# Performance work log

Measured on AMD Instinct MI355X. Metric: run time of the kernel, lower is better.

## Reference

```python
import jax, jax.numpy as jnp
import numpy as np
from jax import lax

# GlobalSeed with a standard Mamba2 (SSD) core.
# C=64 feature channels, G=8 token dim, d_inner=16, d_state=16, nheads=2, headdim=8, d_conv=3.
C_FEAT, G, D_INNER, D_STATE, NHEADS, HEADDIM, D_CONV = 64, 8, 16, 16, 2, 8, 3
CONV_DIM = D_INNER + 2 * D_STATE  # 48
D_IN_PROJ = 2 * D_INNER + 2 * D_STATE + NHEADS  # 66


def setup_inputs() -> dict:
    key = jax.random.key(0)
    ks = jax.random.split(key, 16)
    B, H, W = 16, 128, 128
    s = 0.02
    return {
        "x": jax.random.normal(ks[0], (B, C_FEAT, H, W), jnp.float32),
        "tok_w": s * jax.random.normal(ks[1], (G, C_FEAT), jnp.float32),
        "tok_b": jnp.zeros((G,), jnp.float32),
        "detok_w": s * jax.random.normal(ks[2], (C_FEAT, G), jnp.float32),
        "detok_b": jnp.zeros((C_FEAT,), jnp.float32),
        "in_proj_w": s * jax.random.normal(ks[3], (D_IN_PROJ, G), jnp.float32),
        "in_proj_b": jnp.zeros((D_IN_PROJ,), jnp.float32),
        "conv_w": s * jax.random.normal(ks[4], (CONV_DIM, D_CONV), jnp.float32),
        "conv_b": jnp.zeros((CONV_DIM,), jnp.float32),
        "A_log": jnp.log(jnp.arange(1, NHEADS + 1, dtype=jnp.float32)),
        "D": jnp.ones((NHEADS,), jnp.float32),
        "dt_bias": 0.1 * jax.random.normal(ks[5], (NHEADS,), jnp.float32),
        "norm_w": jnp.ones((D_INNER,), jnp.float32),
        "out_w": s * jax.random.normal(ks[6], (G, D_INNER), jnp.float32),
        "out_b": jnp.zeros((G,), jnp.float32),
    }


def _mamba2(gt, in_proj_w, in_proj_b, conv_w, conv_b, A_log, D, dt_bias, norm_w, out_w, out_b):
    # gt: (B, L, G) tokens
    B, L, _ = gt.shape
    zxbcdt = gt @ in_proj_w.T + in_proj_b  # (B, L, 66)
    z = zxbcdt[..., :D_INNER]
    xBC = zxbcdt[..., D_INNER:D_INNER + CONV_DIM]
    dt = zxbcdt[..., D_INNER + CONV_DIM:]  # (B, L, nheads)
    # depthwise causal conv1d over L
    xBC = lax.conv_general_dilated(
        xBC.transpose(0, 2, 1), conv_w[:, None, :], (1,), [(D_CONV - 1, 0)],
        feature_group_count=CONV_DIM).transpose(0, 2, 1) + conv_b
    xBC = jax.nn.silu(xBC)
    xr = xBC[..., :D_INNER].reshape(B, L, NHEADS, HEADDIM)
    Bm = xBC[..., D_INNER:D_INNER + D_STATE]   # (B, L, N)
    Cm = xBC[..., D_INNER + D_STATE:]          # (B, L, N)
    dt = jax.nn.softplus(dt + dt_bias)          # (B, L, H)
    dec = jnp.exp(dt * (-jnp.exp(A_log)))       # (B, L, H)

    def step(h, inp):
        xt, Bt, Ct, dtt, dct = inp  # (B,H,P) (B,N) (B,N) (B,H) (B,H)
        h = dct[:, :, None, None] * h + (dtt[:, :, None] * xt)[..., None] * Bt[:, None, None, :]
        y = jnp.einsum('bhpn,bn->bhp', h, Ct)
        return h, y

    h0 = jnp.zeros((B, NHEADS, HEADDIM, D_STATE), gt.dtype)
    xs = (xr.transpose(1, 0, 2, 3), Bm.transpose(1, 0, 2), Cm.transpose(1, 0, 2),
          dt.transpose(1, 0, 2), dec.transpose(1, 0, 2))
    _, ys = lax.scan(step, h0, xs)  # (L, B, H, P)
    y = ys.transpose(1, 0, 2, 3) + D[None, None, :, None] * xr
    y = y.reshape(B, L, D_INNER)
    y = y * jax.nn.silu(z)  # gated
    y = y * lax.rsqrt(jnp.mean(y * y, axis=-1, keepdims=True) + 1e-5) * norm_w  # RMSNormGated
    return y @ out_w.T + out_b  # (B, L, G)


def reference(x, tok_w, tok_b, detok_w, detok_b, in_proj_w, in_proj_b, conv_w, conv_b,
              A_log, D, dt_bias, norm_w, out_w, out_b):
    B, C, H, W = x.shape
    L = H * W
    g = jnp.einsum('bchw,gc->bghw', x, tok_w) + tok_b[None, :, None, None]
    gt = g.reshape(B, G, L).transpose(0, 2, 1)  # (B, L, G)
    gt = _mamba2(gt, in_proj_w, in_proj_b, conv_w, conv_b, A_log, D, dt_bias, norm_w, out_w, out_b) + gt
    g2 = gt.transpose(0, 2, 1).reshape(B, G, H, W)
    return x + jnp.einsum('bghw,cg->bchw', g2, detok_w) + detok_b[None, :, None, None]
```

## Files before the change

### kernel.cpp

```cpp
#include <hip/hip_runtime.h>
#include <math.h>

#define NB 16
#define CF 64
#define LL 16384
#define GG 8
#define NH 2
#define CHN 64
#define NCH 256
#define NGRP 16

static constexpr size_t OFF_GT = 0;
static constexpr size_t OFF_U2 = OFF_GT + (size_t)NB*LL*GG;
static constexpr size_t OFF_AC = OFF_U2 + (size_t)NB*NCH*256;
static constexpr size_t OFF_PH = OFF_AC + (size_t)NB*NCH*NH;
static constexpr size_t OFF_CP = OFF_PH + (size_t)NB*NCH*256;
static constexpr size_t OFF_UG = OFF_CP + (size_t)NB*NCH*NH;
static constexpr size_t OFF_AG = OFF_UG + (size_t)NB*NGRP*256;
static constexpr size_t OFF_GH = OFF_AG + (size_t)NB*NGRP*NH;
static constexpr size_t OFF_G2 = OFF_GH + (size_t)NB*NGRP*256;
static constexpr size_t OFF_ST = OFF_G2 + (size_t)NB*LL*GG;
static constexpr size_t WS_FLOATS = OFF_ST + (size_t)NB*NCH*1792;

typedef float f32x4 __attribute__((ext_vector_type(4)));
typedef short bf16x8 __attribute__((ext_vector_type(8)));

__device__ __forceinline__ float siluf(float v){ return v / (1.f + __expf(-v)); }
__device__ __forceinline__ float softplusf(float v){ return v > 20.f ? v : log1pf(__expf(v)); }

__device__ __forceinline__ unsigned short f2bf(float f){
    unsigned int u = __float_as_uint(f);
    u += 0x7fffu + ((u >> 16) & 1u);
    return (unsigned short)(u >> 16);
}
__device__ __forceinline__ float bf2f(unsigned short s){
    return __uint_as_float(((unsigned int)s) << 16);
}
__device__ __forceinline__ unsigned int pack2bf(float lo, float hi){
    return (unsigned int)f2bf(lo) | ((unsigned int)f2bf(hi) << 16);
}
__device__ __forceinline__ unsigned int packtr(float lo, float hi){
    return (__float_as_uint(hi) & 0xffff0000u) | (__float_as_uint(lo) >> 16);
}

__device__ __forceinline__ void load8(float* d, const float* p){
    float4 a = ((const float4*)p)[0];
    float4 b = ((const float4*)p)[1];
    d[0]=a.x; d[1]=a.y; d[2]=a.z; d[3]=a.w;
    d[4]=b.x; d[5]=b.y; d[6]=b.z; d[7]=b.w;
}

__global__ __launch_bounds__(64) void k1a_tok(
    const float* __restrict__ x, const float* __restrict__ tok_w,
    const float* __restrict__ tok_b, float* __restrict__ gtw)
{
    __shared__ float s_tok[GG*CF];
    int tid = threadIdx.x;
    int b  = blockIdx.x >> 6;
    int ck = blockIdx.x & 63;
    int l0 = (ck << 8) + (tid << 2);
    for (int i = tid; i < GG*CF; i += 64) s_tok[i] = tok_w[i];
    __syncthreads();
    float acc[4][GG];
    #pragma unroll
    for (int r = 0; r < 4; ++r)
        #pragma unroll
        for (int g = 0; g < GG; ++g) acc[r][g] = tok_b[g];
    const float* xb = x + (size_t)b*CF*LL + l0;
    #pragma unroll 8
    for (int c = 0; c < CF; ++c) {
        float4 xv = *(const float4*)(xb + (size_t)c*LL);
        float xa[4] = {xv.x, xv.y, xv.z, xv.w};
        #pragma unroll
        for (int g = 0; g < GG; ++g) {
            float w = s_tok[g*CF + c];
            #pragma unroll
            for (int r = 0; r < 4; ++r) acc[r][g] = fmaf(xa[r], w, acc[r][g]);
        }
    }
    float* gp = gtw + ((size_t)b*LL + l0)*GG;
    #pragma unroll
    for (int r = 0; r < 4; ++r) {
        ((float4*)gp)[r*2+0] = make_float4(acc[r][0],acc[r][1],acc[r][2],acc[r][3]);
        ((float4*)gp)[r*2+1] = make_float4(acc[r][4],acc[r][5],acc[r][6],acc[r][7]);
    }
}

__global__ __launch_bounds__(256) void k2a_state(
    const float* __restrict__ gtw,
    const float* __restrict__ ipw, const float* __restrict__ ipb,
    const float* __restrict__ cw, const float* __restrict__ cb,
    const float* __restrict__ A_log, const float* __restrict__ dt_bias,
    float* __restrict__ stw,
    float* __restrict__ U2w, float* __restrict__ Acw)
{
    __shared__ float s_pre[48*68];
    __shared__ float s_xf[64*17], s_bf[64*17], s_cf[64*17];
    __shared__ __align__(16) unsigned short WXbf[16*72];
    __shared__ __align__(16) unsigned short BTbf[16*72];
    __shared__ float s_dt[64][2], s_nda[64][2], s_w[64][2];
    __shared__ float s_ipw[384], s_ipb2[48], s_cw2[144], s_cb2[48], s_wdt[16];

    int tid = threadIdx.x;
    int b = blockIdx.x >> 8, c = blockIdx.x & 255;
    float* stp = stw + ((size_t)(b*NCH + c))*1792;
    for (int i = tid; i < 384; i += 256) s_ipw[i] = ipw[128 + i];
    if (tid < 48) { s_ipb2[tid] = ipb[16 + tid]; s_cb2[tid] = cb[tid]; }
    else if (tid >= 64 && tid < 208) s_cw2[tid - 64] = cw[tid - 64];
    else if (tid >= 224 && tid < 240) s_wdt[tid - 224] = ipw[512 + (tid - 224)];
    __syncthreads();

    float a0e = __expf(A_log[0]), a1e = __expf(A_log[1]);
    float dtb0 = dt_bias[0], dtb1 = dt_bias[1];
    float bdt0 = ipb[64], bdt1 = ipb[65];

    int r = tid >> 2, sub = tid & 3;
    int l = c*CHN + r;
    {
        float g0[8];
        load8(g0, gtw + ((size_t)b*LL + l)*GG);
        #pragma unroll
        for (int k = 0; k < 12; ++k) {
            int ch = sub*12 + k;
            float acc = s_ipb2[ch];
            #pragma unroll
            for (int g = 0; g < 8; ++g) acc = fmaf(g0[g], s_ipw[ch*8+g], acc);
            s_pre[ch*68 + r + 2] = acc;
        }
        if (r < 2) {
            int lh = c*CHN - 1 - r, slot = 1 - r;
            if (lh >= 0) {
                float gh[8];
                load8(gh, gtw + ((size_t)b*LL + lh)*GG);
                #pragma unroll
                for (int k = 0; k < 12; ++k) {
                    int ch = sub*12 + k;
                    float acc = s_ipb2[ch];
                    #pragma unroll
                    for (int g = 0; g < 8; ++g) acc = fmaf(gh[g], s_ipw[ch*8+g], acc);
                    s_pre[ch*68 + slot] = acc;
                }
            } else {
                #pragma unroll
                for (int k = 0; k < 12; ++k) s_pre[(sub*12+k)*68 + slot] = 0.f;
            }
        }
        if (sub == 0) {
            float d0 = bdt0, d1 = bdt1;
            #pragma unroll
            for (int g = 0; g < 8; ++g) {
                d0 = fmaf(g0[g], s_wdt[g],   d0);
                d1 = fmaf(g0[g], s_wdt[8+g], d1);
            }
            float dt0 = softplusf(d0 + dtb0), dt1 = softplusf(d1 + dtb1);
            s_dt[r][0] = dt0; s_dt[r][1] = dt1;
            s_nda[r][0] = -dt0*a0e; s_nda[r][1] = -dt1*a1e;
        }
    }
    __syncthreads();

    {
        #pragma unroll
        for (int k = 0; k < 12; ++k) {
            int ch = sub*12 + k;
            float p0 = s_pre[ch*68 + r];
            float p1 = s_pre[ch*68 + r + 1];
            float p2 = s_pre[ch*68 + r + 2];
            float a = s_cb2[ch];
            a = fmaf(p0, s_cw2[ch*3+0], a);
            a = fmaf(p1, s_cw2[ch*3+1], a);
            a = fmaf(p2, s_cw2[ch*3+2], a);
            float v = siluf(a);
            if (ch < 16)      s_xf[r*17 + ch] = v;
            else if (ch < 32) s_bf[r*17 + (ch-16)] = v;
            else              s_cf[r*17 + (ch-32)] = v;
        }
    }
    if (tid < 64) {
        int rr = tid;
        float v0 = s_nda[rr][0], v1 = s_nda[rr][1];
        #pragma unroll
        for (int off = 1; off < 64; off <<= 1) {
            float t0 = __shfl_up(v0, off);
            float t1 = __shfl_up(v1, off);
            if (rr >= off) { v0 += t0; v1 += t1; }
        }
        float f0 = __shfl(v0, 63), f1 = __shfl(v1, 63);
        s_w[rr][0] = __expf(f0 - v0) * s_dt[rr][0];
        s_w[rr][1] = __expf(f1 - v1) * s_dt[rr][1];
        stp[1536 + rr*2 + 0] = v0;
        stp[1536 + rr*2 + 1] = v1;
        stp[1664 + rr*2 + 0] = s_dt[rr][0];
        stp[1664 + rr*2 + 1] = s_dt[rr][1];
        if (rr == 63)
            *(float2*)(Acw + ((size_t)b*NCH + c)*2) = make_float2(__expf(f0), __expf(f1));
    }
    __syncthreads();

    {
        unsigned int* stX = (unsigned int*)stp;
        unsigned int* stB = (unsigned int*)(stp + 512);
        unsigned int* stC = (unsigned int*)(stp + 1024);
        int half = tid >> 7;
        int t2 = tid & 127;
        int p = t2 & 15, seg = t2 >> 4;
        if (half == 0) {
            unsigned int wdW[4], wdX[4];
            #pragma unroll
            for (int j = 0; j < 4; ++j) {
                int s0 = seg*8 + 2*j, s1 = s0 + 1;
                float x0 = s_xf[s0*17 + p], x1 = s_xf[s1*17 + p];
                wdX[j] = pack2bf(x0, x1);
                wdW[j] = pack2bf(x0 * s_w[s0][p>>3], x1 * s_w[s1][p>>3]);
            }
            *(uint4*)&WXbf[p*72 + seg*8] = make_uint4(wdW[0],wdW[1],wdW[2],wdW[3]);
            *(uint4*)&stX[p*32 + seg*4]  = make_uint4(wdX[0],wdX[1],wdX[2],wdX[3]);
        } else {
            unsigned int wd[4];
            #pragma unroll
            for (int j = 0; j < 4; ++j) {
                int s0 = seg*8 + 2*j, s1 = s0 + 1;
                wd[j] = pack2bf(s_bf[s0*17 + p], s_bf[s1*17 + p]);
            }
            *(uint4*)&BTbf[p*72 + seg*8] = make_uint4(wd[0],wd[1],wd[2],wd[3]);
            int r2 = t2 >> 1, hf = t2 & 1;
            unsigned int wb[4], wc[4];
            #pragma unroll
            for (int j = 0; j < 4; ++j) {
                int c0 = hf*8 + 2*j;
                wb[j] = pack2bf(s_bf[r2*17 + c0], s_bf[r2*17 + c0 + 1]);
                wc[j] = pack2bf(s_cf[r2*17 + c0], s_cf[r2*17 + c0 + 1]);
            }
            *(uint4*)&stB[r2*8 + hf*4] = make_uint4(wb[0],wb[1],wb[2],wb[3]);
            *(uint4*)&stC[r2*8 + hf*4] = make_uint4(wc[0],wc[1],wc[2],wc[3]);
        }
    }
    __syncthreads();

    if (tid < 64) {
        int ar = tid & 15, kb = tid >> 4;
        f32x4 acc = {0.f, 0.f, 0.f, 0.f};
        #pragma unroll
        for (int kk = 0; kk < 2; ++kk) {
            bf16x8 aw = *(const bf16x8*)&WXbf[ar*72 + kk*32 + kb*8];
            bf16x8 bb = *(const bf16x8*)&BTbf[ar*72 + kk*32 + kb*8];
            acc = __builtin_amdgcn_mfma_f32_16x16x32_bf16(aw, bb, acc, 0, 0, 0);
        }
        #pragma unroll
        for (int rg = 0; rg < 4; ++rg)
            U2w[(((size_t)b*NCH + c) << 8) + (kb*4+rg)*16 + ar] = acc[rg];
    }
}

__global__ void k4c1(const float* __restrict__ U2w, const float* __restrict__ Acw,
                     float* __restrict__ phw, float* __restrict__ cpw,
                     float* __restrict__ Ugw, float* __restrict__ Agw)
{
    int b = blockIdx.x >> 4, grp = blockIdx.x & 15;
    int e = threadIdx.x, he = e >> 7;
    size_t base = (size_t)b*NCH + grp*16;
    float u[16], A[16];
    #pragma unroll
    for (int j = 0; j < 16; ++j) u[j] = U2w[((base + j) << 8) + e];
    #pragma unroll
    for (int j = 0; j < 16; ++j) A[j] = Acw[(base + j)*2 + he];
    float h = 0.f, cp = 1.f;
    #pragma unroll
    for (int j = 0; j < 16; ++j) {
        phw[((base + j) << 8) + e] = h;
        if ((e & 127) == 0) cpw[(base + j)*2 + he] = cp;
        h = fmaf(A[j], h, u[j]);
        cp *= A[j];
    }
    Ugw[(((size_t)b*NGRP + grp) << 8) + e] = h;
    if ((e & 127) == 0) Agw[((size_t)b*NGRP + grp)*2 + he] = cp;
}

__global__ void k4c2(const float* __restrict__ Ugw, const float* __restrict__ Agw,
                     float* __restrict__ ghw)
{
    int b = blockIdx.x, e = threadIdx.x, he = e >> 7;
    float u[NGRP], ag[NGRP];
    #pragma unroll
    for (int g = 0; g < NGRP; ++g) {
        u[g]  = Ugw[(((size_t)b*NGRP + g) << 8) + e];
        ag[g] = Agw[((size_t)b*NGRP + g)*2 + he];
    }
    float h = 0.f;
    #pragma unroll
    for (int g = 0; g < NGRP; ++g) {
        ghw[(((size_t)b*NGRP + g) << 8) + e] = h;
        h = fmaf(ag[g], h, u[g]);
    }
}

__global__ __launch_bounds__(256) void k2b_fused(
    const float* __restrict__ gtw,
    const float* __restrict__ ipw, const float* __restrict__ ipb,
    const float* __restrict__ Dv, const float* __restrict__ norm_w,
    const float* __restrict__ out_w, const float* __restrict__ out_b,
    const float* __restrict__ phw, const float* __restrict__ cpw,
    const float* __restrict__ ghw, const float* __restrict__ stw,
    float* __restrict__ g2w)
{
    __shared__ union {
        unsigned short Ct[64*40];
        float yb[64*20];
    } uC;
    __shared__ __align__(16) unsigned short Bt[64*40];
    __shared__ __align__(16) unsigned short XTbf[16*72];
    __shared__ __align__(16) unsigned short M2[2][64*72];
    __shared__ __align__(16) unsigned short Cp0[64*16], Cp1[64*16];
    __shared__ __align__(16) unsigned short hinT[2][8*16];
    __shared__ float s_hin[256];
    __shared__ float s_la[128];
    __shared__ float s_eti[2][64], s_etd[2][64], s_esc[2][4][4];
    __shared__ float s_zw[128], s_ow[128], s_zb[16], s_nw[16], s_ob[8];

    int tid = threadIdx.x;
    int b = blockIdx.x >> 8, c = blockIdx.x & 255;
    const float* stp = stw + ((size_t)(b*NCH + c))*1792;
    const unsigned int* stX = (const unsigned int*)stp;
    const unsigned int* stB = (const unsigned int*)(stp + 512);
    const unsigned int* stC = (const unsigned int*)(stp + 1024);

    int r = tid >> 2, sub = tid & 3;
    float g0[8];
    load8(g0, gtw + ((size_t)b*LL + c*CHN + r)*GG);
    {
        int grp = c >> 4;
        float gh  = ghw[(((size_t)b*NGRP + grp) << 8) + tid];
        float cpv = cpw[((size_t)b*NCH + c)*2 + (tid >> 7)];
        float phv = phw[(((size_t)b*NCH + c) << 8) + tid];
        s_hin[tid] = fmaf(cpv, gh, phv);
    }
    if (tid < 64) {
        int row = tid;
        *(uint4*)&uC.Ct[row*40]      = *(const uint4*)&stC[row*8];
        *(uint4*)&uC.Ct[row*40 + 8]  = *(const uint4*)&stC[row*8 + 4];
        *(uint4*)&uC.Ct[row*40 + 16] = make_uint4(0,0,0,0);
        *(uint4*)&uC.Ct[row*40 + 24] = make_uint4(0,0,0,0);
    } else if (tid < 128) {
        int row = tid - 64;
        *(uint4*)&Bt[row*40]      = *(const uint4*)&stB[row*8];
        *(uint4*)&Bt[row*40 + 8]  = *(const uint4*)&stB[row*8 + 4];
        *(uint4*)&Bt[row*40 + 16] = make_uint4(0,0,0,0);
        *(uint4*)&Bt[row*40 + 24] = make_uint4(0,0,0,0);
    } else {
        int i = tid - 128;
        int p = i >> 3, seg = i & 7;
        *(uint4*)&XTbf[p*72 + seg*8] = *(const uint4*)&stX[p*32 + seg*4];
    }
    if (tid < 128) { s_la[tid] = stp[1536 + tid]; s_zw[tid] = ipw[tid]; }
    else s_ow[tid-128] = out_w[tid-128];
    if (tid < 16) { s_zb[tid] = ipb[tid]; s_nw[tid] = norm_w[tid]; }
    else if (tid < 24) s_ob[tid-16] = out_b[tid-16];
    __syncthreads();

    float D0 = Dv[0], D1 = Dv[1];
    int lane = tid & 63, wv = tid >> 6;
    int ar = lane & 15, kb = lane >> 4;
    int trow = wv*16 + kb*4;

    f32x4 gT[4];
    {
        bf16x8 aC = *(const bf16x8*)&uC.Ct[(wv*16 + ar)*40 + kb*8];
        #pragma unroll
        for (int ss = 0; ss < 4; ++ss) {
            f32x4 g = {0.f, 0.f, 0.f, 0.f};
            if (ss <= wv) {
                bf16x8 bB = *(const bf16x8*)&Bt[(ss*16 + ar)*40 + kb*8];
                g = __builtin_amdgcn_mfma_f32_16x16x32_bf16(aC, bB, g, 0, 0, 0);
            }
            gT[ss] = g;
        }
    }
    if (tid < 128) {
        int h = tid >> 6;
        int rr = (tid & 63);
        float sc = __expf(s_la[rr*2 + h]);
        unsigned short* Cp = h ? Cp1 : Cp0;
        unsigned int* dst = (unsigned int*)&Cp[rr*16];
        #pragma unroll
        for (int j = 0; j < 8; ++j)
            dst[j] = pack2bf(sc * bf2f(uC.Ct[rr*40 + j*2]),
                             sc * bf2f(uC.Ct[rr*40 + j*2 + 1]));
        if (tid < 32) {
            int i = tid;
            int hh = i >> 4, p = (i >> 1) & 7, half = i & 1;
            unsigned int wd[4];
            #pragma unroll
            for (int j = 0; j < 4; ++j)
                wd[j] = pack2bf(s_hin[hh*128 + p*16 + half*8 + 2*j],
                                s_hin[hh*128 + p*16 + half*8 + 2*j + 1]);
            *(uint4*)&hinT[hh][p*16 + half*8] = make_uint4(wd[0],wd[1],wd[2],wd[3]);
        }
    } else {
        int i = tid - 128;
        int h = i >> 6, s = i & 63;
        int anc = s & ~15;
        float d = s_la[anc*2 + h] - s_la[s*2 + h];
        float dtv = stp[1664 + s*2 + h];
        s_eti[h][s] = __expf(-d);
        s_etd[h][s] = __expf(d) * dtv;
        if (i < 32) {
            int h2 = i >> 4, wt = (i >> 2) & 3, ws = i & 3;
            s_esc[h2][wt][ws] = (wt >= ws) ?
                __expf(s_la[(wt*16)*2 + h2] - s_la[(ws*16)*2 + h2]) : 0.f;
        }
    }
    __syncthreads();

    {
        float rowf0[4], rowf1[4];
        #pragma unroll
        for (int rg = 0; rg < 4; ++rg) {
            rowf0[rg] = s_eti[0][trow+rg];
            rowf1[rg] = s_eti[1][trow+rg];
        }
        #pragma unroll
        for (int ss = 0; ss < 4; ++ss) {
            int s = ss*16 + ar;
            if (ss > wv) {
                if (!(ar & 1)) {
                    #pragma unroll
                    for (int rg = 0; rg < 4; ++rg) {
                        *(unsigned int*)&M2[0][(trow+rg)*72 + ss*16 + ar] = 0u;
                        *(unsigned int*)&M2[1][(trow+rg)*72 + ss*16 + ar] = 0u;
                    }
                }
                continue;
            }
            float colf0 = s_esc[0][wv][ss] * s_etd[0][s];
            float colf1 = s_esc[1][wv][ss] * s_etd[1][s];
            #pragma unroll
            for (int rg = 0; rg < 4; ++rg) {
                bool keep = (s <= trow+rg);
                float m0 = keep ? rowf0[rg]*colf0*gT[ss][rg] : 0.f;
                float m1 = keep ? rowf1[rg]*colf1*gT[ss][rg] : 0.f;
                float m0p = __shfl_xor(m0, 1);
                float m1p = __shfl_xor(m1, 1);
                if (!(ar & 1)) {
                    *(unsigned int*)&M2[0][(trow+rg)*72 + ss*16 + ar] = packtr(m0, m0p);
                    *(unsigned int*)&M2[1][(trow+rg)*72 + ss*16 + ar] = packtr(m1, m1p);
                }
            }
        }
    }
    __syncthreads();

    {
        int p = ar;
        f32x4 acc0 = {0.f,0.f,0.f,0.f}, acc1 = {0.f,0.f,0.f,0.f};
        #pragma unroll
        for (int kk = 0; kk < 2; ++kk) {
            bf16x8 am0 = *(const bf16x8*)&M2[0][(wv*16 + ar)*72 + kk*32 + kb*8];
            bf16x8 am1 = *(const bf16x8*)&M2[1][(wv*16 + ar)*72 + kk*32 + kb*8];
            bf16x8 bx0 = {0,0,0,0,0,0,0,0}, bx1 = {0,0,0,0,0,0,0,0};
            if (p < 8) {
                bx0 = *(const bf16x8*)&XTbf[p*72 + kk*32 + kb*8];
                bx1 = *(const bf16x8*)&XTbf[(8+p)*72 + kk*32 + kb*8];
            }
            acc0 = __builtin_amdgcn_mfma_f32_16x16x32_bf16(am0, bx0, acc0, 0, 0, 0);
            acc1 = __builtin_amdgcn_mfma_f32_16x16x32_bf16(am1, bx1, acc1, 0, 0, 0);
        }
        bf16x8 aCp0 = {0,0,0,0,0,0,0,0}, aCp1 = {0,0,0,0,0,0,0,0};
        bf16x8 bh0 = {0,0,0,0,0,0,0,0}, bh1 = {0,0,0,0,0,0,0,0};
        if (kb < 2) {
            aCp0 = *(const bf16x8*)&Cp0[(wv*16 + ar)*16 + kb*8];
            aCp1 = *(const bf16x8*)&Cp1[(wv*16 + ar)*16 + kb*8];
            if (ar < 8) {
                bh0 = *(const bf16x8*)&hinT[0][ar*16 + kb*8];
                bh1 = *(const bf16x8*)&hinT[1][ar*16 + kb*8];
            }
        }
        acc0 = __builtin_amdgcn_mfma_f32_16x16x32_bf16(aCp0, bh0, acc0, 0, 0, 0);
        acc1 = __builtin_amdgcn_mfma_f32_16x16x32_bf16(aCp1, bh1, acc1, 0, 0, 0);
        if (p < 8) {
            #pragma unroll
            for (int rg = 0; rg < 4; ++rg) {
                int t = trow + rg;
                uC.yb[t*20 + p]     = fmaf(D0, bf2f(XTbf[p*72 + t]),     acc0[rg]);
                uC.yb[t*20 + 8 + p] = fmaf(D1, bf2f(XTbf[(8+p)*72 + t]), acc1[rg]);
            }
        }
    }
    __syncthreads();

    {
        int q = sub;
        float vv[4]; float ssq = 0.f;
        #pragma unroll
        for (int j = 0; j < 4; ++j) {
            int hp = q*4 + j;
            float zz = s_zb[hp];
            #pragma unroll
            for (int g = 0; g < 8; ++g) zz = fmaf(g0[g], s_zw[hp*8+g], zz);
            float y = uC.yb[r*20 + hp];
            float w = y * siluf(zz);
            vv[j] = w; ssq = fmaf(w, w, ssq);
        }
        ssq += __shfl_xor(ssq, 1);
        ssq += __shfl_xor(ssq, 2);
        float rn = rsqrtf(ssq*(1.f/16.f) + 1e-5f);
        float o[8];
        #pragma unroll
        for (int g = 0; g < 8; ++g) o[g] = 0.f;
        #pragma unroll
        for (int j = 0; j < 4; ++j) {
            float wj = vv[j] * rn * s_nw[q*4+j];
            #pragma unroll
            for (int g = 0; g < 8; ++g) o[g] = fmaf(wj, s_ow[g*16 + q*4 + j], o[g]);
        }
        #pragma unroll
        for (int g = 0; g < 8; ++g) {
            o[g] += __shfl_xor(o[g], 1);
            o[g] += __shfl_xor(o[g], 2);
        }
        if (q == 0) {
            #pragma unroll
            for (int g = 0; g < 8; ++g) o[g] += s_ob[g] + g0[g];
            float* gp = g2w + ((size_t)b*LL + c*CHN + r)*GG;
            ((float4*)gp)[0] = make_float4(o[0],o[1],o[2],o[3]);
            ((float4*)gp)[1] = make_float4(o[4],o[5],o[6],o[7]);
        }
    }
}

__global__ __launch_bounds__(64) void k5b_detok(
    const float* __restrict__ x, const float* __restrict__ g2w,
    const float* __restrict__ dkw, const float* __restrict__ dkb,
    float* __restrict__ outp)
{
    __shared__ float s_dw[CF*GG];
    __shared__ float s_db[CF];
    int tid = threadIdx.x;
    int b  = blockIdx.x >> 6;
    int ck = blockIdx.x & 63;
    int l0 = (ck << 8) + (tid << 2);
    for (int i = tid; i < CF*GG; i += 64) s_dw[i] = dkw[i];
    s_db[tid] = dkb[tid];
    __syncthreads();
    float g2v[4][8];
    const float* gp = g2w + ((size_t)b*LL + l0)*GG;
    #pragma unroll
    for (int r = 0; r < 4; ++r) load8(g2v[r], gp + r*GG);
    const float* xb = x + (size_t)b*CF*LL + l0;
    float* ob = outp + (size_t)b*CF*LL + l0;
    #pragma unroll 4
    for (int c = 0; c < CF; ++c) {
        float4 xv = *(const float4*)(xb + (size_t)c*LL);
        float bias = s_db[c];
        float oa[4] = {xv.x+bias, xv.y+bias, xv.z+bias, xv.w+bias};
        #pragma unroll
        for (int g = 0; g < GG; ++g) {
            float w = s_dw[c*GG+g];
            #pragma unroll
            for (int r = 0; r < 4; ++r) oa[r] = fmaf(g2v[r][g], w, oa[r]);
        }
        *(float4*)(ob + (size_t)c*LL) = make_float4(oa[0],oa[1],oa[2],oa[3]);
    }
}

extern "C" void kernel_launch(void* const* d_in, const int* in_sizes, int n_in,
                              void* d_out, int out_size, void* d_ws, size_t ws_size,
                              hipStream_t stream) {
    const float* x       = (const float*)d_in[0];
    const float* tok_w   = (const float*)d_in[1];
    const float* tok_b   = (const float*)d_in[2];
    const float* detok_w = (const float*)d_in[3];
    const float* detok_b = (const float*)d_in[4];
    const float* ipw     = (const float*)d_in[5];
    const float* ipb     = (const float*)d_in[6];
    const float* cw      = (const float*)d_in[7];
    const float* cb      = (const float*)d_in[8];
    const float* A_log   = (const float*)d_in[9];
    const float* Dv      = (const float*)d_in[10];
    const float* dt_bias = (const float*)d_in[11];
    const float* norm_w  = (const float*)d_in[12];
    const float* out_w   = (const float*)d_in[13];
    const float* out_b   = (const float*)d_in[14];
    float* ws = (float*)d_ws;
    float* outp = (float*)d_out;

    if (ws_size < WS_FLOATS * sizeof(float)) return;

    k1a_tok<<<NB*64, 64, 0, stream>>>(x, tok_w, tok_b, ws+OFF_GT);
    k2a_state<<<NB*NCH, 256, 0, stream>>>(ws+OFF_GT, ipw, ipb, cw, cb,
        A_log, dt_bias, ws+OFF_ST, ws+OFF_U2, ws+OFF_AC);
    k4c1<<<NB*NGRP, 256, 0, stream>>>(ws+OFF_U2, ws+OFF_AC,
        ws+OFF_PH, ws+OFF_CP, ws+OFF_UG, ws+OFF_AG);
    k4c2<<<NB, 256, 0, stream>>>(ws+OFF_UG, ws+OFF_AG, ws+OFF_GH);
    k2b_fused<<<NB*NCH, 256, 0, stream>>>(ws+OFF_GT, ipw, ipb,
        Dv, norm_w, out_w, out_b,
        ws+OFF_PH, ws+OFF_CP, ws+OFF_GH, ws+OFF_ST, ws+OFF_G2);
    k5b_detok<<<NB*64, 64, 0, stream>>>(x, ws+OFF_G2, detok_w, detok_b, outp);
}
```

Measured before the change: 131.6 us.

## Fold in_proj and causal conv into one MFMA GEMM in k2a_state

```diff
diff --git a/kernel.cpp b/kernel.cpp
--- a/kernel.cpp
+++ b/kernel.cpp
@@ -86,6 +86,42 @@
     }
 }
 
+__device__ __forceinline__ void build_W(
+    int tid, const float* ipw, const float* ipb, const float* cw, const float* cb,
+    unsigned short* Wt, float* s_bias, float* s_c0, float* s_c1, float* s_wdt)
+{
+    int col = tid & 63, kb = tid >> 6;
+    unsigned int wd0=0u, wd1=0u, wd2=0u, wd3=0u;
+    if (col < 48) {
+        if (kb < 3) {
+            float cwv = cw[col*3 + (2-kb)];
+            const float* iprow = ipw + (16+col)*8;
+            wd0 = pack2bf(iprow[0]*cwv, iprow[1]*cwv);
+            wd1 = pack2bf(iprow[2]*cwv, iprow[3]*cwv);
+            wd2 = pack2bf(iprow[4]*cwv, iprow[5]*cwv);
+            wd3 = pack2bf(iprow[6]*cwv, iprow[7]*cwv);
+        }
+    } else if (kb == 0) {
+        const float* iprow = ipw + (col-48)*8;
+        wd0 = pack2bf(iprow[0], iprow[1]);
+        wd1 = pack2bf(iprow[2], iprow[3]);
+        wd2 = pack2bf(iprow[4], iprow[5]);
+        wd3 = pack2bf(iprow[6], iprow[7]);
+    }
+    *(uint4*)&Wt[col*32 + kb*8] = make_uint4(wd0,wd1,wd2,wd3);
+    if (kb == 0) {
+        float bias;
+        if (col < 48) {
+            float w0 = cw[col*3], w1 = cw[col*3+1], w2 = cw[col*3+2];
+            float ib = ipb[16+col];
+            bias = cb[col] + ib*(w0+w1+w2);
+            s_c0[col] = ib*(w0+w1);
+            s_c1[col] = ib*w0;
+        } else bias = ipb[col-48];
+        s_bias[col] = bias;
+    } else if (kb == 1 && col < 16) s_wdt[col] = ipw[512 + col];
+}
+
 __global__ __launch_bounds__(256) void k2a_state(
     const float* __restrict__ gtw,
     const float* __restrict__ ipw, const float* __restrict__ ipb,
@@ -94,88 +130,83 @@
     float* __restrict__ stw,
     float* __restrict__ U2w, float* __restrict__ Acw)
 {
-    __shared__ float s_pre[48*68];
-    __shared__ float s_xf[64*17], s_bf[64*17], s_cf[64*17];
+    __shared__ __align__(16) unsigned short Wt[64*32];
+    __shared__ float s_bias[64], s_c0[48], s_c1[48], s_wdt[16];
+    __shared__ __align__(16) unsigned short XTbf[16*72];
+    __shared__ __align__(16) unsigned short BTbf[16*72];
     __shared__ __align__(16) unsigned short WXbf[16*72];
-    __shared__ __align__(16) unsigned short BTbf[16*72];
+    __shared__ __align__(16) unsigned short Brow[64*16];
+    __shared__ __align__(16) unsigned short Crow[64*16];
     __shared__ float s_dt[64][2], s_nda[64][2], s_w[64][2];
-    __shared__ float s_ipw[384], s_ipb2[48], s_cw2[144], s_cb2[48], s_wdt[16];
 
     int tid = threadIdx.x;
     int b = blockIdx.x >> 8, c = blockIdx.x & 255;
     float* stp = stw + ((size_t)(b*NCH + c))*1792;
-    for (int i = tid; i < 384; i += 256) s_ipw[i] = ipw[128 + i];
-    if (tid < 48) { s_ipb2[tid] = ipb[16 + tid]; s_cb2[tid] = cb[tid]; }
-    else if (tid >= 64 && tid < 208) s_cw2[tid - 64] = cw[tid - 64];
-    else if (tid >= 224 && tid < 240) s_wdt[tid - 224] = ipw[512 + (tid - 224)];
+    build_W(tid, ipw, ipb, cw, cb, Wt, s_bias, s_c0, s_c1, s_wdt);
     __syncthreads();
 
     float a0e = __expf(A_log[0]), a1e = __expf(A_log[1]);
     float dtb0 = dt_bias[0], dtb1 = dt_bias[1];
     float bdt0 = ipb[64], bdt1 = ipb[65];
 
-    int r = tid >> 2, sub = tid & 3;
-    int l = c*CHN + r;
-    {
-        float g0[8];
-        load8(g0, gtw + ((size_t)b*LL + l)*GG);
-        #pragma unroll
-        for (int k = 0; k < 12; ++k) {
-            int ch = sub*12 + k;
-            float acc = s_ipb2[ch];
-            #pragma unroll
-            for (int g = 0; g < 8; ++g) acc = fmaf(g0[g], s_ipw[ch*8+g], acc);
-            s_pre[ch*68 + r + 2] = acc;
-        }
-        if (r < 2) {
-            int lh = c*CHN - 1 - r, slot = 1 - r;
-            if (lh >= 0) {
-                float gh[8];
-                load8(gh, gtw + ((size_t)b*LL + lh)*GG);
-                #pragma unroll
-                for (int k = 0; k < 12; ++k) {
-                    int ch = sub*12 + k;
-                    float acc = s_ipb2[ch];
-                    #pragma unroll
-                    for (int g = 0; g < 8; ++g) acc = fmaf(gh[g], s_ipw[ch*8+g], acc);
-                    s_pre[ch*68 + slot] = acc;
-                }
-            } else {
-                #pragma unroll
-                for (int k = 0; k < 12; ++k) s_pre[(sub*12+k)*68 + slot] = 0.f;
-            }
-        }
-        if (sub == 0) {
-            float d0 = bdt0, d1 = bdt1;
-            #pragma unroll
-            for (int g = 0; g < 8; ++g) {
-                d0 = fmaf(g0[g], s_wdt[g],   d0);
-                d1 = fmaf(g0[g], s_wdt[8+g], d1);
-            }
-            float dt0 = softplusf(d0 + dtb0), dt1 = softplusf(d1 + dtb1);
-            s_dt[r][0] = dt0; s_dt[r][1] = dt1;
-            s_nda[r][0] = -dt0*a0e; s_nda[r][1] = -dt1*a1e;
-        }
-    }
-    __syncthreads();
-
-    {
-        #pragma unroll
-        for (int k = 0; k < 12; ++k) {
-            int ch = sub*12 + k;
-            float p0 = s_pre[ch*68 + r];
-            float p1 = s_pre[ch*68 + r + 1];
-            float p2 = s_pre[ch*68 + r + 2];
-            float a = s_cb2[ch];
-            a = fmaf(p0, s_cw2[ch*3+0], a);
-            a = fmaf(p1, s_cw2[ch*3+1], a);
-            a = fmaf(p2, s_cw2[ch*3+2], a);
-            float v = siluf(a);
-            if (ch < 16)      s_xf[r*17 + ch] = v;
-            else if (ch < 32) s_bf[r*17 + (ch-16)] = v;
-            else              s_cf[r*17 + (ch-32)] = v;
-        }
-    }
+    int lane = tid & 63, wv = tid >> 6;
+    int ar = lane & 15, kb = lane >> 4;
+    int trow = wv*16 + kb*4;
+
+    float fr[8];
+    bf16x8 aop = {0,0,0,0,0,0,0,0};
+    int rowi = c*CHN + wv*16 + ar - kb;
+    if (kb < 3 && rowi >= 0) {
+        load8(fr, gtw + ((size_t)b*LL + rowi)*GG);
+        unsigned int* ap = (unsigned int*)&aop;
+        ap[0] = pack2bf(fr[0],fr[1]); ap[1] = pack2bf(fr[2],fr[3]);
+        ap[2] = pack2bf(fr[4],fr[5]); ap[3] = pack2bf(fr[6],fr[7]);
+    }
+    f32x4 st0, st1, st2;
+    {
+        float b0 = s_bias[ar], b1 = s_bias[16+ar], b2 = s_bias[32+ar];
+        f32x4 c0v = {b0,b0,b0,b0}, c1v = {b1,b1,b1,b1}, c2v = {b2,b2,b2,b2};
+        st0 = __builtin_amdgcn_mfma_f32_16x16x32_bf16(aop, *(const bf16x8*)&Wt[ar*32 + kb*8],      c0v, 0,0,0);
+        st1 = __builtin_amdgcn_mfma_f32_16x16x32_bf16(aop, *(const bf16x8*)&Wt[(16+ar)*32 + kb*8], c1v, 0,0,0);
+        st2 = __builtin_amdgcn_mfma_f32_16x16x32_bf16(aop, *(const bf16x8*)&Wt[(32+ar)*32 + kb*8], c2v, 0,0,0);
+    }
+    if (c == 0 && wv == 0 && kb == 0) {
+        st0[0] -= s_c0[ar];    st0[1] -= s_c1[ar];
+        st1[0] -= s_c0[16+ar]; st1[1] -= s_c1[16+ar];
+        st2[0] -= s_c0[32+ar]; st2[1] -= s_c1[32+ar];
+    }
+    if (kb == 0) {
+        float d0 = bdt0, d1 = bdt1;
+        #pragma unroll
+        for (int g = 0; g < 8; ++g) {
+            d0 = fmaf(fr[g], s_wdt[g],   d0);
+            d1 = fmaf(fr[g], s_wdt[8+g], d1);
+        }
+        float dt0 = softplusf(d0 + dtb0), dt1 = softplusf(d1 + dtb1);
+        int row = wv*16 + ar;
+        s_dt[row][0] = dt0; s_dt[row][1] = dt1;
+        s_nda[row][0] = -dt0*a0e; s_nda[row][1] = -dt1*a1e;
+    }
+    {
+        float v0 = siluf(st0[0]), v1 = siluf(st0[1]), v2 = siluf(st0[2]), v3 = siluf(st0[3]);
+        *(uint2*)&XTbf[ar*72 + trow] = make_uint2(pack2bf(v0,v1), pack2bf(v2,v3));
+        float b0 = siluf(st1[0]), b1 = siluf(st1[1]), b2 = siluf(st1[2]), b3 = siluf(st1[3]);
+        *(uint2*)&BTbf[ar*72 + trow] = make_uint2(pack2bf(b0,b1), pack2bf(b2,b3));
+        float bb[4] = {b0,b1,b2,b3};
+        #pragma unroll
+        for (int rg = 0; rg < 4; ++rg) {
+            float vB = bb[rg];
+            float vC = siluf(st2[rg]);
+            float pB = __shfl_xor(vB, 1);
+            float pC = __shfl_xor(vC, 1);
+            if (!(ar & 1)) {
+                *(unsigned int*)&Brow[(trow+rg)*16 + ar] = pack2bf(vB, pB);
+                *(unsigned int*)&Crow[(trow+rg)*16 + ar] = pack2bf(vC, pC);
+            }
+        }
+    }
+    __syncthreads();
+
     if (tid < 64) {
         int rr = tid;
         float v0 = s_nda[rr][0], v1 = s_nda[rr][1];
@@ -201,54 +232,42 @@
         unsigned int* stX = (unsigned int*)stp;
         unsigned int* stB = (unsigned int*)(stp + 512);
         unsigned int* stC = (unsigned int*)(stp + 1024);
-        int half = tid >> 7;
-        int t2 = tid & 127;
-        int p = t2 & 15, seg = t2 >> 4;
-        if (half == 0) {
-            unsigned int wdW[4], wdX[4];
+        if (tid < 128) {
+            int p = tid >> 3, seg = tid & 7;
+            int s0 = seg*8, he = p >> 3;
+            const unsigned short* xp = &XTbf[p*72 + s0];
+            unsigned int wd[4];
             #pragma unroll
             for (int j = 0; j < 4; ++j) {
-                int s0 = seg*8 + 2*j, s1 = s0 + 1;
-                float x0 = s_xf[s0*17 + p], x1 = s_xf[s1*17 + p];
-                wdX[j] = pack2bf(x0, x1);
-                wdW[j] = pack2bf(x0 * s_w[s0][p>>3], x1 * s_w[s1][p>>3]);
-            }
-            *(uint4*)&WXbf[p*72 + seg*8] = make_uint4(wdW[0],wdW[1],wdW[2],wdW[3]);
-            *(uint4*)&stX[p*32 + seg*4]  = make_uint4(wdX[0],wdX[1],wdX[2],wdX[3]);
+                float lo = bf2f(xp[2*j])   * s_w[s0+2*j][he];
+                float hi = bf2f(xp[2*j+1]) * s_w[s0+2*j+1][he];
+                wd[j] = pack2bf(lo, hi);
+            }
+            *(uint4*)&WXbf[p*72 + s0] = make_uint4(wd[0],wd[1],wd[2],wd[3]);
+            int row = tid >> 1, hf = tid & 1;
+            *(uint4*)&stB[row*8 + hf*4] = *(const uint4*)&Brow[row*16 + hf*8];
         } else {
-            unsigned int wd[4];
-            #pragma unroll
-            for (int j = 0; j < 4; ++j) {
-                int s0 = seg*8 + 2*j, s1 = s0 + 1;
-                wd[j] = pack2bf(s_bf[s0*17 + p], s_bf[s1*17 + p]);
-            }
-            *(uint4*)&BTbf[p*72 + seg*8] = make_uint4(wd[0],wd[1],wd[2],wd[3]);
-            int r2 = t2 >> 1, hf = t2 & 1;
-            unsigned int wb[4], wc[4];
-            #pragma unroll
-            for (int j = 0; j < 4; ++j) {
-                int c0 = hf*8 + 2*j;
-                wb[j] = pack2bf(s_bf[r2*17 + c0], s_bf[r2*17 + c0 + 1]);
-                wc[j] = pack2bf(s_cf[r2*17 + c0], s_cf[r2*17 + c0 + 1]);
-            }
-            *(uint4*)&stB[r2*8 + hf*4] = make_uint4(wb[0],wb[1],wb[2],wb[3]);
-            *(uint4*)&stC[r2*8 + hf*4] = make_uint4(wc[0],wc[1],wc[2],wc[3]);
+            int i = tid - 128;
+            int p = i >> 3, seg = i & 7;
+            *(uint4*)&stX[p*32 + seg*4] = *(const uint4*)&XTbf[p*72 + seg*8];
+            int row = i >> 1, hf = i & 1;
+            *(uint4*)&stC[row*8 + hf*4] = *(const uint4*)&Crow[row*16 + hf*8];
         }
     }
     __syncthreads();
 
     if (tid < 64) {
-        int ar = tid & 15, kb = tid >> 4;
+        int ar2 = tid & 15, kb2 = tid >> 4;
         f32x4 acc = {0.f, 0.f, 0.f, 0.f};
         #pragma unroll
         for (int kk = 0; kk < 2; ++kk) {
-            bf16x8 aw = *(const bf16x8*)&WXbf[ar*72 + kk*32 + kb*8];
-            bf16x8 bb = *(const bf16x8*)&BTbf[ar*72 + kk*32 + kb*8];
+            bf16x8 aw = *(const bf16x8*)&WXbf[ar2*72 + kk*32 + kb2*8];
+            bf16x8 bb = *(const bf16x8*)&BTbf[ar2*72 + kk*32 + kb2*8];
             acc = __builtin_amdgcn_mfma_f32_16x16x32_bf16(aw, bb, acc, 0, 0, 0);
         }
         #pragma unroll
         for (int rg = 0; rg < 4; ++rg)
-            U2w[(((size_t)b*NCH + c) << 8) + (kb*4+rg)*16 + ar] = acc[rg];
+            U2w[(((size_t)b*NCH + c) << 8) + (kb2*4+rg)*16 + ar2] = acc[rg];
     }
 }
 
```

Result: faster. 122.2 us (-7.1%).
